# Performance work log

Hardware: AMD Instinct MI355X
Metric: run time of the kernel (lower is better)

Reference implementation:

```python
import jax, jax.numpy as jnp
import numpy as np

B, C, H, W = 2, 256, 32, 32
NUM_HEADS = 8
HEAD_DIM = C // NUM_HEADS
SCALE = HEAD_DIM ** -0.5
K1, K2 = 2, 3
KERNELS = [3, 5, 7]
STRIDES = [1, 1, 1]
PADS = [1, 2, 3]


def avgpool2d(y, k, s, p):
    # PyTorch AvgPool2d default count_include_pad=True: divide by k*k always
    yp = jnp.pad(y, ((0, 0), (0, 0), (p, p), (p, p)))
    summed = jax.lax.reduce_window(yp, 0.0, jax.lax.add,
                                   (1, 1, k, k), (1, 1, s, s), 'VALID')
    return summed / float(k * k)


def layer_norm(x, g, b, eps=1e-5):
    mu = jnp.mean(x, axis=-1, keepdims=True)
    var = jnp.var(x, axis=-1, keepdims=True)
    return (x - mu) / jnp.sqrt(var + eps) * g + b


def topk_mask(attn, kk):
    # boolean mask with True at the top-kk positions along the last axis
    idx = jax.lax.top_k(attn, kk)[1]                     # [B,h,N,kk]
    mask = jnp.zeros(attn.shape, dtype=bool)
    return jnp.put_along_axis(mask, idx, True, axis=-1, inplace=False)


def setup_inputs() -> dict:
    key = jax.random.key(0)
    ks = jax.random.split(key, 8)
    std = 1.0 / np.sqrt(C)
    return {
        'x': jax.random.normal(ks[0], (B, C, H, W), jnp.float32),
        'y': jax.random.normal(ks[1], (B, C, H, W), jnp.float32),
        'Wq': jax.random.uniform(ks[2], (C, C), jnp.float32, -std, std),
        'Wkv': jax.random.uniform(ks[3], (2 * C, C), jnp.float32, -std, std),
        'Wproj': jax.random.uniform(ks[4], (C, C), jnp.float32, -std, std),
        'bproj': jax.random.uniform(ks[5], (C,), jnp.float32, -std, std),
        'ln_g': jnp.ones((C,), jnp.float32),
        'ln_b': jnp.zeros((C,), jnp.float32),
        'attn1_p': jnp.full((1,), 0.5, jnp.float32),
        'attn2_p': jnp.full((1,), 0.5, jnp.float32),
    }


def reference(x, y, Wq, Wkv, Wproj, bproj, ln_g, ln_b, attn1_p, attn2_p):
    # multi-scale average pooling fusion of y (stride 1 keeps H,W)
    yf = (avgpool2d(y, KERNELS[0], STRIDES[0], PADS[0])
          + avgpool2d(y, KERNELS[1], STRIDES[1], PADS[1])
          + avgpool2d(y, KERNELS[2], STRIDES[2], PADS[2]))
    yf = yf.reshape(B, C, H * W).transpose(0, 2, 1)      # [B, N1, C]
    yf = layer_norm(yf, ln_g, ln_b)
    N1 = yf.shape[1]

    kv = yf @ Wkv.T                                      # [B, N1, 2C]
    kv = kv.reshape(B, N1, 2, NUM_HEADS, HEAD_DIM).transpose(2, 0, 3, 1, 4)
    k, v = kv[0], kv[1]                                  # [B, h, N1, d]

    xf = x.reshape(B, C, H * W).transpose(0, 2, 1)       # [B, N, C]
    N = xf.shape[1]
    q = (xf @ Wq.T).reshape(B, N, NUM_HEADS, HEAD_DIM).transpose(0, 2, 1, 3)

    attn = jnp.einsum('bhnd,bhmd->bhnm', q, k) * SCALE   # [B, h, N, N1]

    neg_inf = jnp.array(-jnp.inf, attn.dtype)
    m1 = topk_mask(attn, int(N1 / K1))
    a1 = jax.nn.softmax(jnp.where(m1, attn, neg_inf), axis=-1)
    out1 = jnp.einsum('bhnm,bhmd->bhnd', a1, v)

    m2 = topk_mask(attn, int(N1 / K2))
    a2 = jax.nn.softmax(jnp.where(m2, attn, neg_inf), axis=-1)
    out2 = jnp.einsum('bhnm,bhmd->bhnd', a2, v)

    out = out1 * attn1_p + out2 * attn2_p                # [B, h, N, d]
    out = out.transpose(0, 2, 1, 3).reshape(B, N, C)
    out = out @ Wproj.T + bproj
    hw = int(np.sqrt(N))
    return out.transpose(0, 2, 1).reshape(B, C, hw, hw)
```

## Files before the change

### kernel.cpp

```cpp
#include <hip/hip_runtime.h>

typedef _Float16 f16;
typedef f16 f16x8 __attribute__((ext_vector_type(8)));
typedef f16 f16x4 __attribute__((ext_vector_type(4)));
typedef float f32x4 __attribute__((ext_vector_type(4)));

constexpr float ATT_SCALE = 0.17677669529663687f;

template<int C> __device__ __forceinline__ float dppadd(float v) {
    return v + __int_as_float(__builtin_amdgcn_update_dpp(0, __float_as_int(v), C, 0xf, 0xf, true));
}
template<int C> __device__ __forceinline__ float dppmax(float v) {
    return fmaxf(v, __int_as_float(__builtin_amdgcn_update_dpp(__float_as_int(v), __float_as_int(v), C, 0xf, 0xf, false)));
}
__device__ __forceinline__ float wave_sum(float v) {
    v = dppadd<0x111>(v); v = dppadd<0x112>(v); v = dppadd<0x114>(v); v = dppadd<0x118>(v);
    v = dppadd<0x142>(v); v = dppadd<0x143>(v);
    return __int_as_float(__builtin_amdgcn_readlane(__float_as_int(v), 63));
}
__device__ __forceinline__ float wave_max(float v) {
    v = dppmax<0x111>(v); v = dppmax<0x112>(v); v = dppmax<0x114>(v); v = dppmax<0x118>(v);
    v = dppmax<0x142>(v); v = dppmax<0x143>(v);
    return __int_as_float(__builtin_amdgcn_readlane(__float_as_int(v), 63));
}

__global__ __launch_bounds__(256) void prep_kernel(const float* __restrict__ y,
                                                   float* __restrict__ pooled,
                                                   const float* __restrict__ x,
                                                   f16* __restrict__ xT,
                                                   const float* __restrict__ Wq,
                                                   const float* __restrict__ Wkv,
                                                   const float* __restrict__ Wp,
                                                   f16* __restrict__ wq16,
                                                   f16* __restrict__ wkv16,
                                                   f16* __restrict__ wp16)
{
    __shared__ float sh[1444];
    int bid = blockIdx.x, t = threadIdx.x;
    if (bid < 512) {
        float (*p)[38] = (float(*)[38])sh;
        const float* plane = y + (size_t)bid * 1024;
        for (int i = t; i < 38 * 38; i += 256) (&p[0][0])[i] = 0.f;
        __syncthreads();
        for (int i = t; i < 1024; i += 256) p[(i >> 5) + 3][(i & 31) + 3] = plane[i];
        __syncthreads();
        int b = bid >> 8, c = bid & 255;
        for (int i = t; i < 1024; i += 256) {
            int r = (i >> 5) + 3, cc = (i & 31) + 3;
            float s3 = 0.f;
            #pragma unroll
            for (int dr = -1; dr <= 1; ++dr)
                #pragma unroll
                for (int dc = -1; dc <= 1; ++dc) s3 += p[r + dr][cc + dc];
            float r5 = 0.f;
            #pragma unroll
            for (int dc = -2; dc <= 2; ++dc) r5 += p[r - 2][cc + dc] + p[r + 2][cc + dc];
            #pragma unroll
            for (int dr = -1; dr <= 1; ++dr) r5 += p[r + dr][cc - 2] + p[r + dr][cc + 2];
            float r7 = 0.f;
            #pragma unroll
            for (int dc = -3; dc <= 3; ++dc) r7 += p[r - 3][cc + dc] + p[r + 3][cc + dc];
            #pragma unroll
            for (int dr = -2; dr <= 2; ++dr) r7 += p[r + dr][cc - 3] + p[r + dr][cc + 3];
            float s5 = s3 + r5, s7 = s5 + r7;
            pooled[((size_t)b * 1024 + i) * 256 + c] =
                s3 * (1.f / 9.f) + s5 * (1.f / 25.f) + s7 * (1.f / 49.f);
        }
    } else if (bid < 1024) {
        float (*tile)[33] = (float(*)[33])sh;
        int id = bid - 512;
        int b = id >> 8, ct = (id >> 5) & 7, nt = id & 31;
        int rr = t >> 5, j = t & 31;
        #pragma unroll
        for (int r = rr; r < 32; r += 8)
            tile[r][j] = x[((size_t)b * 256 + ct * 32 + r) * 1024 + nt * 32 + j];
        __syncthreads();
        #pragma unroll
        for (int r = rr; r < 32; r += 8)
            xT[((size_t)b * 1024 + nt * 32 + r) * 256 + ct * 32 + j] = (f16)tile[j][r];
    } else {
        int i = (bid - 1024) * 256 + t;
        if (i < 65536) { wq16[i] = (f16)Wq[i]; wp16[i] = (f16)Wp[i]; }
        wkv16[i] = (f16)Wkv[i];
    }
}

__device__ __forceinline__ void gemm_tile(const f16* __restrict__ A, const f16* __restrict__ Bm,
                                          int row0, int ncol0, int l15, int lhi, f32x4 acc[4])
{
    for (int k0 = 0; k0 < 256; k0 += 32) {
        f16x8 a = *(const f16x8*)(A + (size_t)(row0 + l15) * 256 + k0 + lhi * 8);
        #pragma unroll
        for (int j = 0; j < 4; ++j) {
            f16x8 bf = *(const f16x8*)(Bm + (size_t)(ncol0 + j * 16 + l15) * 256 + k0 + lhi * 8);
            acc[j] = __builtin_amdgcn_mfma_f32_16x16x32_f16(a, bf, acc[j], 0, 0, 0);
        }
    }
}

__global__ __launch_bounds__(256) void qkv_kernel(const f16* __restrict__ xT,
                                                  const float* __restrict__ pooled,
                                                  const float* __restrict__ lng,
                                                  const float* __restrict__ lnb,
                                                  const f16* __restrict__ wq16,
                                                  const f16* __restrict__ wkv16,
                                                  f16* __restrict__ q16,
                                                  f16* __restrict__ k16,
                                                  f16* __restrict__ vT16)
{
    __shared__ f16 At[64 * 256];
    int w = threadIdx.x >> 6, lane = threadIdx.x & 63;
    int l15 = lane & 15, lhi = lane >> 4;
    if (blockIdx.x < 128) {
        int mt = blockIdx.x >> 2, nt = blockIdx.x & 3;
        int row0 = mt * 64 + w * 16;
        f32x4 acc[4] = {};
        gemm_tile(xT, wq16, row0, nt * 64, l15, lhi, acc);
        #pragma unroll
        for (int j = 0; j < 4; ++j) {
            int col = nt * 64 + j * 16 + l15;
            int h = col >> 5, d = col & 31;
            #pragma unroll
            for (int r = 0; r < 4; ++r) {
                int row = row0 + 4 * lhi + r;
                int b = row >> 10, n = row & 1023;
                q16[(((size_t)(b * 8 + h)) * 1024 + n) * 32 + d] = (f16)(acc[j][r] * ATT_SCALE);
            }
        }
    } else {
        int bid = blockIdx.x - 128;
        int mt = bid >> 3, nt = bid & 7;
        int row0g = mt * 64;
        float4 gg = ((const float4*)lng)[lane];
        float4 bb = ((const float4*)lnb)[lane];
        for (int rr = 0; rr < 16; ++rr) {
            int r = w * 16 + rr;
            float4 v = *(const float4*)(pooled + (size_t)(row0g + r) * 256 + lane * 4);
            float su = v.x + v.y + v.z + v.w;
            float s2 = v.x * v.x + v.y * v.y + v.z * v.z + v.w * v.w;
            su = wave_sum(su); s2 = wave_sum(s2);
            float muv = su * (1.f / 256.f);
            float rstd = rsqrtf(s2 * (1.f / 256.f) - muv * muv + 1e-5f);
            f16x4 o;
            o[0] = (f16)((v.x - muv) * rstd * gg.x + bb.x);
            o[1] = (f16)((v.y - muv) * rstd * gg.y + bb.y);
            o[2] = (f16)((v.z - muv) * rstd * gg.z + bb.z);
            o[3] = (f16)((v.w - muv) * rstd * gg.w + bb.w);
            *(f16x4*)(At + r * 256 + ((lane * 4) ^ ((r & 7) << 3))) = o;
        }
        __syncthreads();
        f32x4 acc[4] = {};
        int a_r = w * 16 + l15;
        int asw = (a_r & 7) << 3;
        for (int k0 = 0; k0 < 256; k0 += 32) {
            f16x8 a = *(const f16x8*)(At + a_r * 256 + ((k0 + lhi * 8) ^ asw));
            #pragma unroll
            for (int j = 0; j < 4; ++j) {
                f16x8 bf = *(const f16x8*)(wkv16 + (size_t)(nt * 64 + j * 16 + l15) * 256 + k0 + lhi * 8);
                acc[j] = __builtin_amdgcn_mfma_f32_16x16x32_f16(a, bf, acc[j], 0, 0, 0);
            }
        }
        #pragma unroll
        for (int j = 0; j < 4; ++j) {
            int col = nt * 64 + j * 16 + l15;
            #pragma unroll
            for (int r = 0; r < 4; ++r) {
                int row = row0g + w * 16 + 4 * lhi + r;
                int b = row >> 10, n = row & 1023;
                float v = acc[j][r];
                if (col < 256) {
                    int h = col >> 5, d = col & 31;
                    k16[(((size_t)(b * 8 + h)) * 1024 + n) * 32 + d] = (f16)v;
                } else {
                    int c2 = col - 256, h = c2 >> 5, d = c2 & 31;
                    vT16[(((size_t)(b * 8 + h)) * 32 + d) * 1024 + n] = (f16)v;
                }
            }
        }
    }
}

__device__ __forceinline__ int cnt16(const float* s, float m)
{
    int c = 0;
    #pragma unroll
    for (int i = 0; i < 16; ++i)
        c += (int)__popcll(__ballot(s[i] >= m));
    return c;
}

#define WIDEN(sarr, aa, bb, K, mn4, mxv, lo, hi, cl, ch) { \
    int _ca = cnt16(sarr, (aa)); int _cb = cnt16(sarr, (bb)); \
    bool _lm = _ca < (K); bool _hm = _cb > (K); \
    lo = _lm ? (mn4) : (_hm ? (bb) : (aa)); \
    hi = _lm ? (aa)  : (_hm ? (mxv) : (bb)); \
    cl = _lm ? 1024.f : (_hm ? (float)_cb : (float)_ca); \
    ch = _lm ? (float)_ca : (_hm ? 1.f : (float)_cb); }

#define MID(it, lo, hi, cl, ch, K, m) { \
    if ((it) & 1) { m = 0.5f * (lo + hi); } \
    else { float _den = fmaxf(cl - ch, 1.0f); \
        m = lo + (hi - lo) * (cl - (float)(K)) * __builtin_amdgcn_rcpf(_den); \
        float _mg = 0.12f * (hi - lo); \
        m = fminf(fmaxf(m, lo + _mg), hi - _mg); } }

#define UPD(cv, K, lo, hi, cl, ch, m) { bool _g = (cv) >= (K); \
    lo = _g ? (m) : lo; cl = _g ? (float)(cv) : cl; \
    hi = _g ? hi : (m); ch = _g ? ch : (float)(cv); }

__global__ __launch_bounds__(512, 4) void attn_kernel(const f16* __restrict__ q16,
                                                      const f16* __restrict__ k16,
                                                      const f16* __restrict__ vT16,
                                                      const float* __restrict__ a1p,
                                                      const float* __restrict__ a2p,
                                                      f16* __restrict__ oat)
{
    __shared__ f16 Sb[16 * 1024];
    int bid = blockIdx.x;
    int bh = bid >> 6, rb = bid & 63;
    int row0 = rb * 16;
    int w = threadIdx.x >> 6, lane = threadIdx.x & 63;
    int l15 = lane & 15, lhi = lane >> 4;
    const f16* Qb = q16 + (size_t)bh * 32768;
    const f16* Kb = k16 + (size_t)bh * 32768;
    const f16* Vb = vT16 + (size_t)bh * 32768;

    {
        f16x8 qf = *(const f16x8*)(Qb + (size_t)(row0 + l15) * 32 + lhi * 8);
        int q = l15, sw1 = q & 7;
        int phalf = (lhi & 1) * 4;
        #pragma unroll
        for (int j = 0; j < 8; ++j) {
            int c0 = w * 128 + j * 16;
            f16x8 kf = *(const f16x8*)(Kb + (size_t)(c0 + l15) * 32 + lhi * 8);
            f32x4 z = {0.f, 0.f, 0.f, 0.f};
            f32x4 d = __builtin_amdgcn_mfma_f32_16x16x32_f16(kf, qf, z, 0, 0, 0);
            int pl = (c0 >> 3) + (lhi >> 1);
            int pp = pl ^ sw1;
            f16x4 hv;
            hv[0] = (f16)d[0]; hv[1] = (f16)d[1]; hv[2] = (f16)d[2]; hv[3] = (f16)d[3];
            *(f16x4*)(Sb + q * 1024 + pp * 8 + phalf) = hv;
        }
    }
    __syncthreads();

    float c_a1 = a1p[0], c_a2 = a2p[0];
    int r0 = 2 * w, r1 = r0 + 1;
    int cs0 = r0 & 7, cs1 = r1 & 7;
    float s0[16], s1[16];
    {
        f16x8 ha = *(const f16x8*)(Sb + r0 * 1024 + ((lane ^ cs0) << 3));
        f16x8 hb = *(const f16x8*)(Sb + r0 * 1024 + (((64 + lane) ^ cs0) << 3));
        f16x8 hc = *(const f16x8*)(Sb + r1 * 1024 + ((lane ^ cs1) << 3));
        f16x8 hd = *(const f16x8*)(Sb + r1 * 1024 + (((64 + lane) ^ cs1) << 3));
        #pragma unroll
        for (int i = 0; i < 8; ++i) {
            s0[i] = (float)ha[i]; s0[8 + i] = (float)hb[i];
            s1[i] = (float)hc[i]; s1[8 + i] = (float)hd[i];
        }
    }
    float mx0l = s0[0], mx1l = s1[0];
    float su0 = 0.f, q0 = 0.f, su1 = 0.f, q1 = 0.f;
    #pragma unroll
    for (int i = 0; i < 16; ++i) {
        mx0l = fmaxf(mx0l, s0[i]); su0 += s0[i]; q0 = fmaf(s0[i], s0[i], q0);
        mx1l = fmaxf(mx1l, s1[i]); su1 += s1[i]; q1 = fmaf(s1[i], s1[i], q1);
    }
    float mx0 = wave_max(mx0l), mx1 = wave_max(mx1l);
    float mu0 = wave_sum(su0) * (1.f / 1024.f), mu1 = wave_sum(su1) * (1.f / 1024.f);
    float sg0 = sqrtf(fmaxf(wave_sum(q0) * (1.f / 1024.f) - mu0 * mu0, 1e-30f));
    float sg1 = sqrtf(fmaxf(wave_sum(q1) * (1.f / 1024.f) - mu1 * mu1, 1e-30f));

    float lo1, hi1, cl1, ch1, lo2, hi2, cl2, ch2;
    float lo3, hi3, cl3, ch3, lo4, hi4, cl4, ch4;
    {
        float d0 = 0.25f * sg0, d1 = 0.25f * sg1;
        float g0 = mu0 + 0.4316f * sg0, g1 = mu1 + 0.4316f * sg1;
        float mn40 = mu0 - 4.f * sg0, mn41 = mu1 - 4.f * sg1;
        WIDEN(s0, mu0 - d0, mu0 + d0, 512, mn40, mx0, lo1, hi1, cl1, ch1);
        WIDEN(s0, g0 - d0,  g0 + d0,  341, mn40, mx0, lo2, hi2, cl2, ch2);
        WIDEN(s1, mu1 - d1, mu1 + d1, 512, mn41, mx1, lo3, hi3, cl3, ch3);
        WIDEN(s1, g1 - d1,  g1 + d1,  341, mn41, mx1, lo4, hi4, cl4, ch4);
    }
    #pragma unroll
    for (int it = 0; it < 8; ++it) {
        float m1, m2, m3, m4;
        MID(it, lo1, hi1, cl1, ch1, 512, m1);
        MID(it, lo2, hi2, cl2, ch2, 341, m2);
        MID(it, lo3, hi3, cl3, ch3, 512, m3);
        MID(it, lo4, hi4, cl4, ch4, 341, m4);
        int c1 = cnt16(s0, m1);
        int c2 = cnt16(s0, m2);
        int c3 = cnt16(s1, m3);
        int c4 = cnt16(s1, m4);
        UPD(c1, 512, lo1, hi1, cl1, ch1, m1);
        UPD(c2, 341, lo2, hi2, cl2, ch2, m2);
        UPD(c3, 512, lo3, hi3, cl3, ch3, m3);
        UPD(c4, 341, lo4, hi4, cl4, ch4, m4);
    }
    {
        float t1a[16], t2a[16];
        float l1 = 0.f, l2 = 0.f;
        #pragma unroll
        for (int i = 0; i < 16; ++i) {
            float ev = __expf(s0[i] - mx0);
            float u1 = (s0[i] >= lo1) ? ev : 0.f;
            float u2 = (s0[i] >= lo2) ? ev : 0.f;
            t1a[i] = u1; t2a[i] = u2;
            l1 += u1; l2 += u2;
        }
        l1 = wave_sum(l1); l2 = wave_sum(l2);
        float w1 = c_a1 / l1, w2 = c_a2 / l2;
        f16x8 oa, ob;
        #pragma unroll
        for (int i = 0; i < 8; ++i) {
            oa[i] = (f16)(t1a[i] * w1 + t2a[i] * w2);
            ob[i] = (f16)(t1a[8 + i] * w1 + t2a[8 + i] * w2);
        }
        *(f16x8*)(Sb + r0 * 1024 + ((lane ^ cs0) << 3)) = oa;
        *(f16x8*)(Sb + r0 * 1024 + (((64 + lane) ^ cs0) << 3)) = ob;
    }
    {
        float t1b[16], t2b[16];
        float l3 = 0.f, l4 = 0.f;
        #pragma unroll
        for (int i = 0; i < 16; ++i) {
            float ev = __expf(s1[i] - mx1);
            float u1 = (s1[i] >= lo3) ? ev : 0.f;
            float u2 = (s1[i] >= lo4) ? ev : 0.f;
            t1b[i] = u1; t2b[i] = u2;
            l3 += u1; l4 += u2;
        }
        l3 = wave_sum(l3); l4 = wave_sum(l4);
        float w3 = c_a1 / l3, w4 = c_a2 / l4;
        f16x8 oc, od;
        #pragma unroll
        for (int i = 0; i < 8; ++i) {
            oc[i] = (f16)(t1b[i] * w3 + t2b[i] * w4);
            od[i] = (f16)(t1b[8 + i] * w3 + t2b[8 + i] * w4);
        }
        *(f16x8*)(Sb + r1 * 1024 + ((lane ^ cs1) << 3)) = oc;
        *(f16x8*)(Sb + r1 * 1024 + (((64 + lane) ^ cs1) << 3)) = od;
    }
    __syncthreads();

    f32x4 acc0 = {}, acc1 = {};
    #pragma unroll
    for (int ks = 0; ks < 4; ++ks) {
        int pl = w * 16 + ks * 4 + lhi;
        int pp = pl ^ (l15 & 7);
        f16x8 af = *(const f16x8*)(Sb + l15 * 1024 + (pp << 3));
        int m0 = w * 128 + ks * 32 + lhi * 8;
        f16x8 b0 = *(const f16x8*)(Vb + (size_t)l15 * 1024 + m0);
        f16x8 b1v = *(const f16x8*)(Vb + (size_t)(16 + l15) * 1024 + m0);
        acc0 = __builtin_amdgcn_mfma_f32_16x16x32_f16(af, b0, acc0, 0, 0, 0);
        acc1 = __builtin_amdgcn_mfma_f32_16x16x32_f16(af, b1v, acc1, 0, 0, 0);
    }
    __syncthreads();
    float* Pf = (float*)Sb;
    #pragma unroll
    for (int r2 = 0; r2 < 4; ++r2) {
        int rw = 4 * lhi + r2;
        Pf[w * 512 + rw * 32 + l15]      = acc0[r2];
        Pf[w * 512 + rw * 32 + 16 + l15] = acc1[r2];
    }
    __syncthreads();
    if (threadIdx.x < 128) {
        int o4 = threadIdx.x << 2;
        float4 v = *(const float4*)&Pf[o4];
        #pragma unroll
        for (int ww = 1; ww < 8; ++ww) {
            float4 p = *(const float4*)&Pf[ww * 512 + o4];
            v.x += p.x; v.y += p.y; v.z += p.z; v.w += p.w;
        }
        int rr = o4 >> 5, d0 = o4 & 31;
        int b = bh >> 3, h = bh & 7;
        f16x4 o;
        o[0] = (f16)v.x; o[1] = (f16)v.y; o[2] = (f16)v.z; o[3] = (f16)v.w;
        *(f16x4*)(oat + ((size_t)b * 1024 + row0 + rr) * 256 + h * 32 + d0) = o;
    }
}

__global__ __launch_bounds__(256) void projgemm_kernel(const f16* __restrict__ A,
                                                       const f16* __restrict__ Bm,
                                                       const float* __restrict__ bias,
                                                       float* __restrict__ out)
{
    __shared__ float tile[64][65];
    int mt = blockIdx.x >> 2, nt = blockIdx.x & 3;
    int w = threadIdx.x >> 6, lane = threadIdx.x & 63;
    int l15 = lane & 15, lhi = lane >> 4;
    int row0 = mt * 64 + w * 16;
    f32x4 acc[4] = {};
    gemm_tile(A, Bm, row0, nt * 64, l15, lhi, acc);
    #pragma unroll
    for (int j = 0; j < 4; ++j) {
        int col_l = j * 16 + l15;
        float bv = bias[nt * 64 + col_l];
        #pragma unroll
        for (int r = 0; r < 4; ++r)
            tile[col_l][w * 16 + 4 * lhi + r] = acc[j][r] + bv;
    }
    __syncthreads();
    int b = (mt * 64) >> 10, n0 = (mt * 64) & 1023;
    int col_l = threadIdx.x >> 2, part = threadIdx.x & 3;
    size_t base = (size_t)b * 262144 + (size_t)(nt * 64 + col_l) * 1024 + n0 + part * 16;
    #pragma unroll
    for (int q = 0; q < 4; ++q) {
        float4 v;
        v.x = tile[col_l][part * 16 + q * 4 + 0];
        v.y = tile[col_l][part * 16 + q * 4 + 1];
        v.z = tile[col_l][part * 16 + q * 4 + 2];
        v.w = tile[col_l][part * 16 + q * 4 + 3];
        *(float4*)(out + base + q * 4) = v;
    }
}

extern "C" void kernel_launch(void* const* d_in, const int* in_sizes, int n_in,
                              void* d_out, int out_size, void* d_ws, size_t ws_size,
                              hipStream_t stream)
{
    const float* x     = (const float*)d_in[0];
    const float* y     = (const float*)d_in[1];
    const float* Wq    = (const float*)d_in[2];
    const float* Wkv   = (const float*)d_in[3];
    const float* Wproj = (const float*)d_in[4];
    const float* bproj = (const float*)d_in[5];
    const float* ln_g  = (const float*)d_in[6];
    const float* ln_b  = (const float*)d_in[7];
    const float* a1p   = (const float*)d_in[8];
    const float* a2p   = (const float*)d_in[9];
    float* out = (float*)d_out;

    char* wsb = (char*)d_ws;
    float* pooled = (float*)(wsb);
    f16* xT    = (f16*)(wsb + ((size_t)2 << 20));
    f16* wq16  = (f16*)(wsb + ((size_t)3 << 20));
    f16* wkv16 = (f16*)(wsb + ((size_t)3 << 20) + (128 << 10));
    f16* wp16  = (f16*)(wsb + ((size_t)3 << 20) + (384 << 10));
    f16* q16   = (f16*)(wsb + ((size_t)3 << 20) + (512 << 10));
    f16* k16   = (f16*)(wsb + ((size_t)3 << 20) + (512 << 10) + ((size_t)1 << 20));
    f16* vT16  = (f16*)(wsb + ((size_t)3 << 20) + (512 << 10) + ((size_t)2 << 20));
    f16* oat   = (f16*)(wsb + ((size_t)3 << 20) + (512 << 10) + ((size_t)3 << 20));

    prep_kernel<<<1536, 256, 0, stream>>>(y, pooled, x, xT, Wq, Wkv, Wproj,
                                          wq16, wkv16, wp16);
    qkv_kernel<<<384, 256, 0, stream>>>(xT, pooled, ln_g, ln_b, wq16, wkv16,
                                        q16, k16, vT16);
    attn_kernel<<<1024, 512, 0, stream>>>(q16, k16, vT16, a1p, a2p, oat);
    projgemm_kernel<<<128, 256, 0, stream>>>(oat, wp16, bproj, out);
}
```

Before: 69.11 us.

## Fold LayerNorm into KV weights, use exp2 softmax, raise attn occupancy

LayerNorm is folded algebraically into the KV projection. gamma is premultiplied into the f16 Wkv, per-output sums of W·gamma and W·beta are precomputed, and qkv applies the mean and rstd correction in the epilogue. This removes the normalize-to-LDS staging pass, and A is read straight from pooled fp32 and converted to f16 in registers. The attention softmax moves to exp2 with pre-scaled log2e scores and recomputes exponentials rather than holding two 16-element arrays, which cuts register pressure. Launch bounds change from 4 to 6 waves per EU. The cost is some extra exp work, plus precision risk from feeding un-normalized fp32 pooled values to f16 before the correction.

New measurement: 82.29 us. 1.19x slower.

```diff
diff --git a/kernel.cpp b/kernel.cpp
--- a/kernel.cpp
+++ b/kernel.cpp
@@ -6,6 +6,7 @@
 typedef float f32x4 __attribute__((ext_vector_type(4)));
 
 constexpr float ATT_SCALE = 0.17677669529663687f;
+constexpr float LOG2E = 1.4426950408889634f;
 
 template<int C> __device__ __forceinline__ float dppadd(float v) {
     return v + __int_as_float(__builtin_amdgcn_update_dpp(0, __float_as_int(v), C, 0xf, 0xf, true));
@@ -31,9 +32,13 @@
                                                    const float* __restrict__ Wq,
                                                    const float* __restrict__ Wkv,
                                                    const float* __restrict__ Wp,
+                                                   const float* __restrict__ lng,
+                                                   const float* __restrict__ lnb,
                                                    f16* __restrict__ wq16,
                                                    f16* __restrict__ wkv16,
-                                                   f16* __restrict__ wp16)
+                                                   f16* __restrict__ wp16,
+                                                   float* __restrict__ sg,
+                                                   float* __restrict__ sb)
 {
     __shared__ float sh[1444];
     int bid = blockIdx.x, t = threadIdx.x;
@@ -78,10 +83,23 @@
         #pragma unroll
         for (int r = rr; r < 32; r += 8)
             xT[((size_t)b * 1024 + nt * 32 + r) * 256 + ct * 32 + j] = (f16)tile[j][r];
-    } else {
+    } else if (bid < 1536) {
         int i = (bid - 1024) * 256 + t;
         if (i < 65536) { wq16[i] = (f16)Wq[i]; wp16[i] = (f16)Wp[i]; }
-        wkv16[i] = (f16)Wkv[i];
+        wkv16[i] = (f16)(Wkv[i] * lng[i & 255]);
+    } else {
+        int o = (bid - 1536) * 256 + t;
+        const float4* wr = (const float4*)(Wkv + (size_t)o * 256);
+        const float4* gr = (const float4*)lng;
+        const float4* br = (const float4*)lnb;
+        float sgs = 0.f, sbs = 0.f;
+        #pragma unroll 8
+        for (int c4 = 0; c4 < 64; ++c4) {
+            float4 wv = wr[c4], gv = gr[c4], bv = br[c4];
+            sgs += wv.x * gv.x + wv.y * gv.y + wv.z * gv.z + wv.w * gv.w;
+            sbs += wv.x * bv.x + wv.y * bv.y + wv.z * bv.z + wv.w * bv.w;
+        }
+        sg[o] = sgs; sb[o] = sbs;
     }
 }
 
@@ -100,15 +118,14 @@
 
 __global__ __launch_bounds__(256) void qkv_kernel(const f16* __restrict__ xT,
                                                   const float* __restrict__ pooled,
-                                                  const float* __restrict__ lng,
-                                                  const float* __restrict__ lnb,
                                                   const f16* __restrict__ wq16,
                                                   const f16* __restrict__ wkv16,
+                                                  const float* __restrict__ sg,
+                                                  const float* __restrict__ sb,
                                                   f16* __restrict__ q16,
                                                   f16* __restrict__ k16,
                                                   f16* __restrict__ vT16)
 {
-    __shared__ f16 At[64 * 256];
     int w = threadIdx.x >> 6, lane = threadIdx.x & 63;
     int l15 = lane & 15, lhi = lane >> 4;
     if (blockIdx.x < 128) {
@@ -128,46 +145,62 @@
             }
         }
     } else {
+        __shared__ float st_part[64][4][2];
+        __shared__ float stats[64][2];
         int bid = blockIdx.x - 128;
         int mt = bid >> 3, nt = bid & 7;
         int row0g = mt * 64;
-        float4 gg = ((const float4*)lng)[lane];
-        float4 bb = ((const float4*)lnb)[lane];
-        for (int rr = 0; rr < 16; ++rr) {
-            int r = w * 16 + rr;
-            float4 v = *(const float4*)(pooled + (size_t)(row0g + r) * 256 + lane * 4);
-            float su = v.x + v.y + v.z + v.w;
-            float s2 = v.x * v.x + v.y * v.y + v.z * v.z + v.w * v.w;
-            su = wave_sum(su); s2 = wave_sum(s2);
-            float muv = su * (1.f / 256.f);
-            float rstd = rsqrtf(s2 * (1.f / 256.f) - muv * muv + 1e-5f);
-            f16x4 o;
-            o[0] = (f16)((v.x - muv) * rstd * gg.x + bb.x);
-            o[1] = (f16)((v.y - muv) * rstd * gg.y + bb.y);
-            o[2] = (f16)((v.z - muv) * rstd * gg.z + bb.z);
-            o[3] = (f16)((v.w - muv) * rstd * gg.w + bb.w);
-            *(f16x4*)(At + r * 256 + ((lane * 4) ^ ((r & 7) << 3))) = o;
+        {
+            int row = threadIdx.x >> 2, part = threadIdx.x & 3;
+            const float4* pr = (const float4*)(pooled + (size_t)(row0g + row) * 256 + part * 64);
+            float su = 0.f, qq = 0.f;
+            #pragma unroll
+            for (int i = 0; i < 16; ++i) {
+                float4 v = pr[i];
+                su += v.x + v.y + v.z + v.w;
+                qq += v.x * v.x + v.y * v.y + v.z * v.z + v.w * v.w;
+            }
+            st_part[row][part][0] = su; st_part[row][part][1] = qq;
+        }
+        __syncthreads();
+        if (threadIdx.x < 64) {
+            int row = threadIdx.x;
+            float su = st_part[row][0][0] + st_part[row][1][0] + st_part[row][2][0] + st_part[row][3][0];
+            float qq = st_part[row][0][1] + st_part[row][1][1] + st_part[row][2][1] + st_part[row][3][1];
+            float mu = su * (1.f / 256.f);
+            float rstd = rsqrtf(qq * (1.f / 256.f) - mu * mu + 1e-5f);
+            stats[row][0] = mu; stats[row][1] = rstd;
         }
         __syncthreads();
         f32x4 acc[4] = {};
-        int a_r = w * 16 + l15;
-        int asw = (a_r & 7) << 3;
+        const float* Ap = pooled + (size_t)(row0g + w * 16 + l15) * 256;
         for (int k0 = 0; k0 < 256; k0 += 32) {
-            f16x8 a = *(const f16x8*)(At + a_r * 256 + ((k0 + lhi * 8) ^ asw));
+            float4 u0 = *(const float4*)(Ap + k0 + lhi * 8);
+            float4 u1 = *(const float4*)(Ap + k0 + lhi * 8 + 4);
+            f16x8 a;
+            a[0] = (f16)u0.x; a[1] = (f16)u0.y; a[2] = (f16)u0.z; a[3] = (f16)u0.w;
+            a[4] = (f16)u1.x; a[5] = (f16)u1.y; a[6] = (f16)u1.z; a[7] = (f16)u1.w;
             #pragma unroll
             for (int j = 0; j < 4; ++j) {
                 f16x8 bf = *(const f16x8*)(wkv16 + (size_t)(nt * 64 + j * 16 + l15) * 256 + k0 + lhi * 8);
                 acc[j] = __builtin_amdgcn_mfma_f32_16x16x32_f16(a, bf, acc[j], 0, 0, 0);
             }
         }
+        float mu_r[4], rs_r[4];
+        #pragma unroll
+        for (int r = 0; r < 4; ++r) {
+            int lr = w * 16 + 4 * lhi + r;
+            mu_r[r] = stats[lr][0]; rs_r[r] = stats[lr][1];
+        }
         #pragma unroll
         for (int j = 0; j < 4; ++j) {
             int col = nt * 64 + j * 16 + l15;
+            float sgv = sg[col], sbv = sb[col];
             #pragma unroll
             for (int r = 0; r < 4; ++r) {
                 int row = row0g + w * 16 + 4 * lhi + r;
                 int b = row >> 10, n = row & 1023;
-                float v = acc[j][r];
+                float v = rs_r[r] * acc[j][r] - rs_r[r] * mu_r[r] * sgv + sbv;
                 if (col < 256) {
                     int h = col >> 5, d = col & 31;
                     k16[(((size_t)(b * 8 + h)) * 1024 + n) * 32 + d] = (f16)v;
@@ -208,7 +241,7 @@
     lo = _g ? (m) : lo; cl = _g ? (float)(cv) : cl; \
     hi = _g ? hi : (m); ch = _g ? ch : (float)(cv); }
 
-__global__ __launch_bounds__(512, 4) void attn_kernel(const f16* __restrict__ q16,
+__global__ __launch_bounds__(512, 6) void attn_kernel(const f16* __restrict__ q16,
                                                       const f16* __restrict__ k16,
                                                       const f16* __restrict__ vT16,
                                                       const float* __restrict__ a1p,
@@ -255,8 +288,8 @@
         f16x8 hd = *(const f16x8*)(Sb + r1 * 1024 + (((64 + lane) ^ cs1) << 3));
         #pragma unroll
         for (int i = 0; i < 8; ++i) {
-            s0[i] = (float)ha[i]; s0[8 + i] = (float)hb[i];
-            s1[i] = (float)hc[i]; s1[8 + i] = (float)hd[i];
+            s0[i] = (float)ha[i] * LOG2E; s0[8 + i] = (float)hb[i] * LOG2E;
+            s1[i] = (float)hc[i] * LOG2E; s1[8 + i] = (float)hd[i] * LOG2E;
         }
     }
     float mx0l = s0[0], mx1l = s1[0];
@@ -299,45 +332,47 @@
         UPD(c4, 341, lo4, hi4, cl4, ch4, m4);
     }
     {
-        float t1a[16], t2a[16];
         float l1 = 0.f, l2 = 0.f;
         #pragma unroll
         for (int i = 0; i < 16; ++i) {
-            float ev = __expf(s0[i] - mx0);
-            float u1 = (s0[i] >= lo1) ? ev : 0.f;
-            float u2 = (s0[i] >= lo2) ? ev : 0.f;
-            t1a[i] = u1; t2a[i] = u2;
-            l1 += u1; l2 += u2;
+            float ev = exp2f(s0[i] - mx0);
+            l1 += (s0[i] >= lo1) ? ev : 0.f;
+            l2 += (s0[i] >= lo2) ? ev : 0.f;
         }
         l1 = wave_sum(l1); l2 = wave_sum(l2);
         float w1 = c_a1 / l1, w2 = c_a2 / l2;
         f16x8 oa, ob;
         #pragma unroll
         for (int i = 0; i < 8; ++i) {
-            oa[i] = (f16)(t1a[i] * w1 + t2a[i] * w2);
-            ob[i] = (f16)(t1a[8 + i] * w1 + t2a[8 + i] * w2);
+            float ev = exp2f(s0[i] - mx0);
+            float wt = (s0[i] >= lo1 ? w1 : 0.f) + (s0[i] >= lo2 ? w2 : 0.f);
+            oa[i] = (f16)(ev * wt);
+            float ev2 = exp2f(s0[8 + i] - mx0);
+            float wt2 = (s0[8 + i] >= lo1 ? w1 : 0.f) + (s0[8 + i] >= lo2 ? w2 : 0.f);
+            ob[i] = (f16)(ev2 * wt2);
         }
         *(f16x8*)(Sb + r0 * 1024 + ((lane ^ cs0) << 3)) = oa;
         *(f16x8*)(Sb + r0 * 1024 + (((64 + lane) ^ cs0) << 3)) = ob;
     }
     {
-        float t1b[16], t2b[16];
         float l3 = 0.f, l4 = 0.f;
         #pragma unroll
         for (int i = 0; i < 16; ++i) {
-            float ev = __expf(s1[i] - mx1);
-            float u1 = (s1[i] >= lo3) ? ev : 0.f;
-            float u2 = (s1[i] >= lo4) ? ev : 0.f;
-            t1b[i] = u1; t2b[i] = u2;
-            l3 += u1; l4 += u2;
+            float ev = exp2f(s1[i] - mx1);
+            l3 += (s1[i] >= lo3) ? ev : 0.f;
+            l4 += (s1[i] >= lo4) ? ev : 0.f;
         }
         l3 = wave_sum(l3); l4 = wave_sum(l4);
         float w3 = c_a1 / l3, w4 = c_a2 / l4;
         f16x8 oc, od;
         #pragma unroll
         for (int i = 0; i < 8; ++i) {
-            oc[i] = (f16)(t1b[i] * w3 + t2b[i] * w4);
-            od[i] = (f16)(t1b[8 + i] * w3 + t2b[8 + i] * w4);
+            float ev = exp2f(s1[i] - mx1);
+            float wt = (s1[i] >= lo3 ? w3 : 0.f) + (s1[i] >= lo4 ? w4 : 0.f);
+            oc[i] = (f16)(ev * wt);
+            float ev2 = exp2f(s1[8 + i] - mx1);
+            float wt2 = (s1[8 + i] >= lo3 ? w3 : 0.f) + (s1[8 + i] >= lo4 ? w4 : 0.f);
+            od[i] = (f16)(ev2 * wt2);
         }
         *(f16x8*)(Sb + r1 * 1024 + ((lane ^ cs1) << 3)) = oc;
         *(f16x8*)(Sb + r1 * 1024 + (((64 + lane) ^ cs1) << 3)) = od;
@@ -442,10 +477,12 @@
     f16* k16   = (f16*)(wsb + ((size_t)3 << 20) + (512 << 10) + ((size_t)1 << 20));
     f16* vT16  = (f16*)(wsb + ((size_t)3 << 20) + (512 << 10) + ((size_t)2 << 20));
     f16* oat   = (f16*)(wsb + ((size_t)3 << 20) + (512 << 10) + ((size_t)3 << 20));
-
-    prep_kernel<<<1536, 256, 0, stream>>>(y, pooled, x, xT, Wq, Wkv, Wproj,
-                                          wq16, wkv16, wp16);
-    qkv_kernel<<<384, 256, 0, stream>>>(xT, pooled, ln_g, ln_b, wq16, wkv16,
+    float* sgp = (float*)(wsb + ((size_t)3 << 20) + (512 << 10) + ((size_t)4 << 20));
+    float* sbp = sgp + 512;
+
+    prep_kernel<<<1538, 256, 0, stream>>>(y, pooled, x, xT, Wq, Wkv, Wproj,
+                                          ln_g, ln_b, wq16, wkv16, wp16, sgp, sbp);
+    qkv_kernel<<<384, 256, 0, stream>>>(xT, pooled, wq16, wkv16, sgp, sbp,
                                         q16, k16, vT16);
     attn_kernel<<<1024, 512, 0, stream>>>(q16, k16, vT16, a1p, a2p, oat);
     projgemm_kernel<<<128, 256, 0, stream>>>(oat, wp16, bproj, out);
```
